# Kernel optimization log

Hardware: AMD Instinct MI355X
Metric: run time of the kernel (lower is better)

## Reference

```python
import jax, jax.numpy as jnp
import numpy as np

N_HEADS = 16
HEAD_DIM = 64
DIM = 1024
B, L = 2, 2048


def setup_inputs() -> dict:
    key = jax.random.key(0)
    ks = jax.random.split(key, 6)
    s = 1.0 / np.sqrt(DIM)
    return {
        "X": jax.random.normal(ks[0], (B, L, DIM), dtype=jnp.float32),
        "attention_mask": jax.random.randint(ks[1], (B, L, L), 0, 2, dtype=jnp.int32),
        "Wq": jax.random.normal(ks[2], (DIM, DIM), dtype=jnp.float32) * s,
        "Wk": jax.random.normal(ks[3], (DIM, DIM), dtype=jnp.float32) * s,
        "Wv": jax.random.normal(ks[4], (DIM, DIM), dtype=jnp.float32) * s,
        "Wo": jax.random.normal(ks[5], (DIM, DIM), dtype=jnp.float32) * s,
    }


def reference(X, attention_mask, Wq, Wk, Wv, Wo):
    # Linear weights follow torch convention: (out_features, in_features)
    b, l, _ = X.shape
    Q = (X @ Wq.T).reshape(b, l, N_HEADS, HEAD_DIM).transpose(0, 2, 1, 3)  # [B,H,L,D]
    K = (X @ Wk.T).reshape(b, l, N_HEADS, HEAD_DIM).transpose(0, 2, 1, 3)
    V = (X @ Wv.T).reshape(b, l, N_HEADS, HEAD_DIM).transpose(0, 2, 1, 3)
    scores = jnp.einsum("bhqd,bhkd->bhqk", Q, K) / np.sqrt(HEAD_DIM)  # [B,H,L,L]
    mask = (attention_mask[:, None, :, :] == 0)  # broadcast over heads
    scores = jnp.where(mask, jnp.float32(-1e20), scores)
    probs = jax.nn.softmax(scores, axis=-1)
    # dropout is identity in eval/inference mode
    ctx = jnp.einsum("bhqk,bhkd->bhqd", probs, V)  # [B,H,L,D]
    ctx = ctx.transpose(0, 2, 1, 3).reshape(b, l, N_HEADS * HEAD_DIM)
    return ctx @ Wo.T
```

## Files before the change

kernel.cpp:

```cpp
#include <hip/hip_runtime.h>
#include <cstddef>


typedef __bf16 bf16x8 __attribute__((ext_vector_type(8)));
typedef __bf16 bf16x4 __attribute__((ext_vector_type(4)));
typedef float  f32x4  __attribute__((ext_vector_type(4)));
typedef short  s16x4  __attribute__((ext_vector_type(4)));

__device__ __forceinline__ void async16(const __bf16* g, __bf16* l) {
  __builtin_amdgcn_global_load_lds((const __attribute__((address_space(1))) unsigned int*)g,
                                   (__attribute__((address_space(3))) unsigned int*)l, 16, 0, 0);
}

__global__ __launch_bounds__(256) void cvt_all(
    const float* __restrict__ X,  const float* __restrict__ Wq, const float* __restrict__ Wk,
    const float* __restrict__ Wv, const float* __restrict__ Wo,
    __bf16* __restrict__ oX,  __bf16* __restrict__ oWq, __bf16* __restrict__ oWk,
    __bf16* __restrict__ oWv, __bf16* __restrict__ oWo) {
  int i = blockIdx.x * 256 + threadIdx.x;
  const float* s; __bf16* d; int off;
  if (i < 1048576)      { s = X;  d = oX;  off = i; }
  else if (i < 1310720) { s = Wq; d = oWq; off = i - 1048576; }
  else if (i < 1572864) { s = Wk; d = oWk; off = i - 1310720; }
  else if (i < 1835008) { s = Wv; d = oWv; off = i - 1572864; }
  else                  { s = Wo; d = oWo; off = i - 1835008; }
  float4 v = ((const float4*)s)[off];
  bf16x4 o;
  o.x = (__bf16)v.x; o.y = (__bf16)v.y; o.z = (__bf16)v.z; o.w = (__bf16)v.w;
  ((bf16x4*)d)[off] = o;
}

__global__ __launch_bounds__(256) void mask_pack(const int* __restrict__ m,
                                                 unsigned long long* __restrict__ pm) {
  int w = blockIdx.x * 4 + (threadIdx.x >> 6);
  int lane = threadIdx.x & 63;
  unsigned long long bits = __ballot(m[(size_t)w * 64 + lane] != 0);
  int b = w >> 16, q = (w >> 5) & 2047, kt = w & 31;
  if (lane == 0) pm[((size_t)b << 16) + kt * 2048 + q] = bits;
}

template<bool OUT_BF16>
__device__ __forceinline__ void gemm128(const __bf16* __restrict__ A, const __bf16* __restrict__ B,
                                        void* __restrict__ C, int lda, int ldb, int ldc,
                                        int m0, int n0, __bf16* As, __bf16* Bs) {
  const int tid = threadIdx.x;
  const int wave = tid >> 6, lane = tid & 63, quad = lane >> 4, l15 = lane & 15;
  const int wm = (wave & 1) * 64, wn = (wave >> 1) * 64;
  const f32x4 z4 = {0.f, 0.f, 0.f, 0.f};
  f32x4 acc[4][4];
#pragma unroll
  for (int i = 0; i < 4; ++i)
#pragma unroll
    for (int j = 0; j < 4; ++j) acc[i][j] = z4;

  for (int k0 = 0; k0 < 1024; k0 += 32) {
#pragma unroll
    for (int s = 0; s < 2; ++s) {
      int p = (wave * 2 + s) * 64 + lane;
      int r = p >> 2;
      int cc = (p & 3) ^ ((r >> 1) & 3);
      async16(A + (size_t)(m0 + r) * lda + (k0 + cc * 8), As + (wave * 2 + s) * 512);
      async16(B + (size_t)(n0 + r) * ldb + (k0 + cc * 8), Bs + (wave * 2 + s) * 512);
    }
    __syncthreads();
    bf16x8 af[4], bfr[4];
#pragma unroll
    for (int i = 0; i < 4; ++i) {
      int r = wm + i * 16 + l15;
      int cc = quad ^ ((r >> 1) & 3);
      af[i] = *(const bf16x8*)(As + r * 32 + cc * 8);
    }
#pragma unroll
    for (int j = 0; j < 4; ++j) {
      int r = wn + j * 16 + l15;
      int cc = quad ^ ((r >> 1) & 3);
      bfr[j] = *(const bf16x8*)(Bs + r * 32 + cc * 8);
    }
#pragma unroll
    for (int i = 0; i < 4; ++i)
#pragma unroll
      for (int j = 0; j < 4; ++j)
        acc[i][j] = __builtin_amdgcn_mfma_f32_16x16x32_bf16(af[i], bfr[j], acc[i][j], 0, 0, 0);
    __syncthreads();
  }
#pragma unroll
  for (int i = 0; i < 4; ++i)
#pragma unroll
    for (int j = 0; j < 4; ++j)
#pragma unroll
      for (int rr = 0; rr < 4; ++rr) {
        int row = m0 + wm + i * 16 + quad * 4 + rr;
        int col = n0 + wn + j * 16 + l15;
        if (OUT_BF16) ((__bf16*)C)[(size_t)row * ldc + col] = (__bf16)acc[i][j][rr];
        else          ((float*)C)[(size_t)row * ldc + col]  = acc[i][j][rr];
      }
}

__global__ __launch_bounds__(256) void qkv_gemm(const __bf16* __restrict__ X,
                                                const __bf16* __restrict__ Wq,
                                                const __bf16* __restrict__ Wk,
                                                const __bf16* __restrict__ Wv,
                                                __bf16* __restrict__ Q, __bf16* __restrict__ K,
                                                __bf16* __restrict__ Vt) {
  __shared__ __bf16 As[4096], Bs[4096];
  int t = blockIdx.x, z = blockIdx.y;
  if (z < 2) {
    int mt = t & 31, nt = t >> 5;
    gemm128<true>(X, z ? Wk : Wq, z ? K : Q, 1024, 1024, 1024, mt * 128, nt * 128, As, Bs);
  } else {
    int mt = t & 7, nt = t >> 3;
    gemm128<true>(Wv, X, Vt, 1024, 1024, 4096, mt * 128, nt * 128, As, Bs);
  }
}

__global__ __launch_bounds__(256) void out_gemm(const __bf16* __restrict__ Ctx,
                                                const __bf16* __restrict__ Wo,
                                                float* __restrict__ Out) {
  __shared__ __bf16 As[4096], Bs[4096];
  int t = blockIdx.x;
  int mt = t & 31, nt = t >> 5;
  gemm128<false>(Ctx, Wo, Out, 1024, 1024, 1024, mt * 128, nt * 128, As, Bs);
}

__global__ __launch_bounds__(256, 2) void attn_kernel(
    const __bf16* __restrict__ Q, const __bf16* __restrict__ K,
    const __bf16* __restrict__ Vt, const unsigned long long* __restrict__ pm,
    __bf16* __restrict__ Ctx) {
  __shared__ __bf16 Ks[2][4096];
  __shared__ __bf16 Vs[2][4096];
  const int tid = threadIdx.x;
  const int wave = tid >> 6, lane = tid & 63, quad = lane >> 4, l15 = lane & 15;
  const int id = blockIdx.x;
  const int qt = id >> 5, hb = id & 31, h = hb & 15, b = hb >> 4;
  const int q0 = qt * 128;
  const int qw = q0 + wave * 32;

  bf16x8 aq[2][2];
#pragma unroll
  for (int st = 0; st < 2; ++st) {
    const __bf16* Qp = Q + (size_t)(b * 2048 + qw + st * 16 + l15) * 1024 + h * 64 + quad * 8;
    aq[st][0] = *(const bf16x8*)Qp;
    aq[st][1] = *(const bf16x8*)(Qp + 32);
  }

  const unsigned long long* Pm = pm + ((size_t)b << 16) + qw + l15;

  auto stage = [&](int buf, int kv0) {
#pragma unroll
    for (int s = 0; s < 2; ++s) {
      int p = s * 256 + wave * 64 + lane;
      int r = p >> 3, c = (p & 7) ^ (r & 7);
      async16(K  + (size_t)(b * 2048 + kv0 + r) * 1024 + h * 64 + c * 8,
              &Ks[buf][(s * 256 + wave * 64) * 8]);
      async16(Vt + (size_t)(h * 64 + r) * 4096 + b * 2048 + kv0 + c * 8,
              &Vs[buf][(s * 256 + wave * 64) * 8]);
    }
  };

  stage(0, 0);
  unsigned long long mw[2] = {Pm[0], Pm[16]};

  const f32x4 z4 = {0.f, 0.f, 0.f, 0.f};
  const short one_bf16 = (short)0x3F80;
  const s16x4 vOnes = {one_bf16, one_bf16, one_bf16, one_bf16};
  f32x4 acc[2][4];
#pragma unroll
  for (int st = 0; st < 2; ++st)
#pragma unroll
    for (int dt = 0; dt < 4; ++dt) acc[st][dt] = z4;
  f32x4 acc_l[2] = {z4, z4};

  for (int t = 0; t < 32; ++t) {
    __syncthreads();
    if (t < 31) stage((t & 1) ^ 1, (t + 1) * 64);

    const __bf16* Kc = Ks[t & 1];
    const __bf16* Vc = Vs[t & 1];

    bf16x8 kA[8];
#pragma unroll
    for (int jt = 0; jt < 4; ++jt) {
      int r = jt * 16 + l15;
      kA[jt * 2]     = *(const bf16x8*)(Kc + r * 64 + ((quad ^ (r & 7)) * 8));
      kA[jt * 2 + 1] = *(const bf16x8*)(Kc + r * 64 + (((4 + quad) ^ (r & 7)) * 8));
    }
    s16x4 vB[4][4];
#pragma unroll
    for (int dt = 0; dt < 4; ++dt) {
      int d = dt * 16 + l15;
#pragma unroll
      for (int kf = 0; kf < 4; ++kf)
        vB[dt][kf] = *(const s16x4*)(Vc + d * 64 + (((kf * 2 + (quad >> 1)) ^ (d & 7)) * 8)
                                     + (quad & 1) * 4);
    }

#pragma unroll
    for (int st = 0; st < 2; ++st) {
      f32x4 s4[4];
#pragma unroll
      for (int jt = 0; jt < 4; ++jt) {
        f32x4 tt = z4;
        tt = __builtin_amdgcn_mfma_f32_16x16x32_bf16(kA[jt * 2],     aq[st][0], tt, 0, 0, 0);
        tt = __builtin_amdgcn_mfma_f32_16x16x32_bf16(kA[jt * 2 + 1], aq[st][1], tt, 0, 0, 0);
        s4[jt] = tt;
      }

      unsigned long long wq = mw[st] >> (quad * 4);
      if (t < 31) mw[st] = Pm[(size_t)(t + 1) * 2048 + st * 16];
      unsigned lo32 = (unsigned)wq, hi32 = (unsigned)(wq >> 32);

#pragma unroll
      for (int kf = 0; kf < 4; ++kf) {
        unsigned bw = (kf < 2) ? lo32 : hi32;
        s16x4 ptk;
#pragma unroll
        for (int rr = 0; rr < 4; ++rr) {
          float e = fmaf(s4[kf][rr], 0.18033688011112042f, -28.853900817779268f);
          e = (bw & (1u << ((kf & 1) * 16 + rr))) ? e : -1e30f;
          float pv = __builtin_amdgcn_exp2f(e);
          ptk[rr] = __builtin_bit_cast(short, (__bf16)pv);
        }
        acc_l[st] = __builtin_amdgcn_mfma_f32_16x16x16bf16_1k(ptk, vOnes, acc_l[st], 0, 0, 0);
#pragma unroll
        for (int dt = 0; dt < 4; ++dt)
          acc[st][dt] = __builtin_amdgcn_mfma_f32_16x16x16bf16_1k(ptk, vB[dt][kf], acc[st][dt], 0, 0, 0);
      }
    }
  }

#pragma unroll
  for (int st = 0; st < 2; ++st) {
    f32x4 inv;
#pragma unroll
    for (int rr = 0; rr < 4; ++rr) inv[rr] = 1.0f / acc_l[st][rr];
#pragma unroll
    for (int dt = 0; dt < 4; ++dt)
#pragma unroll
      for (int rr = 0; rr < 4; ++rr)
        Ctx[(size_t)(b * 2048 + qw + st * 16 + quad * 4 + rr) * 1024 + h * 64 + dt * 16 + l15] =
            (__bf16)(acc[st][dt][rr] * inv[rr]);
  }
}

extern "C" void kernel_launch(void* const* d_in, const int* in_sizes, int n_in,
                              void* d_out, int out_size, void* d_ws, size_t ws_size,
                              hipStream_t stream) {
  const float* X  = (const float*)d_in[0];
  const int* mask = (const int*)d_in[1];
  const float* Wq = (const float*)d_in[2];
  const float* Wk = (const float*)d_in[3];
  const float* Wv = (const float*)d_in[4];
  const float* Wo = (const float*)d_in[5];

  __bf16* w   = (__bf16*)d_ws;
  __bf16* Xbf = w;
  __bf16* Wqb = Xbf + 4194304;
  __bf16* Wkb = Wqb + 1048576;
  __bf16* Wvb = Wkb + 1048576;
  __bf16* Wob = Wvb + 1048576;
  __bf16* Qb  = Wob + 1048576;
  __bf16* Kb  = Qb + 4194304;
  __bf16* Vtb = Kb + 4194304;
  __bf16* Ctx = Vtb + 4194304;
  unsigned long long* pmt = (unsigned long long*)Wqb;

  cvt_all<<<8192, 256, 0, stream>>>(X, Wq, Wk, Wv, Wo, Xbf, Wqb, Wkb, Wvb, Wob);
  qkv_gemm<<<dim3(256, 3), 256, 0, stream>>>(Xbf, Wqb, Wkb, Wvb, Qb, Kb, Vtb);
  mask_pack<<<32768, 256, 0, stream>>>(mask, pmt);
  attn_kernel<<<512, 256, 0, stream>>>(Qb, Kb, Vtb, pmt, Ctx);
  out_gemm<<<256, 256, 0, stream>>>(Ctx, Wob, (float*)d_out);
}
```

Before: 234.6 us.

## Split attention KV range in two blocks and merge partial outputs

Splits each attention block's 2048-key loop into two halves, doubling the grid to 1024 blocks and raising launch bounds to 4 blocks per CU. Each half writes its unnormalized context and row sums, and a new merge kernel adds the halves and normalizes. The softmax scale is folded into Wq during conversion and the exponent bias goes into the MFMA accumulator init, which removes one FMA per score. This trades more parallelism and occupancy for an extra kernel launch, extra global traffic, and bf16 rounding of the partial sums.

```diff
diff --git a/kernel.cpp b/kernel.cpp
--- a/kernel.cpp
+++ b/kernel.cpp
@@ -18,15 +18,16 @@
     __bf16* __restrict__ oX,  __bf16* __restrict__ oWq, __bf16* __restrict__ oWk,
     __bf16* __restrict__ oWv, __bf16* __restrict__ oWo) {
   int i = blockIdx.x * 256 + threadIdx.x;
-  const float* s; __bf16* d; int off;
+  const float* s; __bf16* d; int off; float sc = 1.0f;
   if (i < 1048576)      { s = X;  d = oX;  off = i; }
-  else if (i < 1310720) { s = Wq; d = oWq; off = i - 1048576; }
+  else if (i < 1310720) { s = Wq; d = oWq; off = i - 1048576; sc = 0.18033688011112042f; }
   else if (i < 1572864) { s = Wk; d = oWk; off = i - 1310720; }
   else if (i < 1835008) { s = Wv; d = oWv; off = i - 1572864; }
   else                  { s = Wo; d = oWo; off = i - 1835008; }
   float4 v = ((const float4*)s)[off];
   bf16x4 o;
-  o.x = (__bf16)v.x; o.y = (__bf16)v.y; o.z = (__bf16)v.z; o.w = (__bf16)v.w;
+  o.x = (__bf16)(v.x * sc); o.y = (__bf16)(v.y * sc);
+  o.z = (__bf16)(v.z * sc); o.w = (__bf16)(v.w * sc);
   ((bf16x4*)d)[off] = o;
 }
 
@@ -122,18 +123,20 @@
   gemm128<false>(Ctx, Wo, Out, 1024, 1024, 1024, mt * 128, nt * 128, As, Bs);
 }
 
-__global__ __launch_bounds__(256, 2) void attn_kernel(
+__global__ __launch_bounds__(256, 4) void attn_kernel(
     const __bf16* __restrict__ Q, const __bf16* __restrict__ K,
     const __bf16* __restrict__ Vt, const unsigned long long* __restrict__ pm,
-    __bf16* __restrict__ Ctx) {
+    __bf16* __restrict__ c0, __bf16* __restrict__ c1, float* __restrict__ lp) {
   __shared__ __bf16 Ks[2][4096];
   __shared__ __bf16 Vs[2][4096];
   const int tid = threadIdx.x;
   const int wave = tid >> 6, lane = tid & 63, quad = lane >> 4, l15 = lane & 15;
   const int id = blockIdx.x;
-  const int qt = id >> 5, hb = id & 31, h = hb & 15, b = hb >> 4;
+  const int hb = id & 31, h = hb & 15, b = hb >> 4;
+  const int kvh = (id >> 5) & 1, qt = id >> 6;
   const int q0 = qt * 128;
   const int qw = q0 + wave * 32;
+  const int kt0 = kvh * 16;
 
   bf16x8 aq[2][2];
 #pragma unroll
@@ -157,10 +160,12 @@
     }
   };
 
-  stage(0, 0);
-  unsigned long long mw[2] = {Pm[0], Pm[16]};
+  stage(0, kt0 * 64);
+  unsigned long long mw[2] = {Pm[(size_t)kt0 * 2048], Pm[(size_t)kt0 * 2048 + 16]};
 
   const f32x4 z4 = {0.f, 0.f, 0.f, 0.f};
+  const f32x4 cbias = {-28.853900817779268f, -28.853900817779268f,
+                       -28.853900817779268f, -28.853900817779268f};
   const short one_bf16 = (short)0x3F80;
   const s16x4 vOnes = {one_bf16, one_bf16, one_bf16, one_bf16};
   f32x4 acc[2][4];
@@ -170,9 +175,9 @@
     for (int dt = 0; dt < 4; ++dt) acc[st][dt] = z4;
   f32x4 acc_l[2] = {z4, z4};
 
-  for (int t = 0; t < 32; ++t) {
+  for (int t = 0; t < 16; ++t) {
     __syncthreads();
-    if (t < 31) stage((t & 1) ^ 1, (t + 1) * 64);
+    if (t < 15) stage((t & 1) ^ 1, (kt0 + t + 1) * 64);
 
     const __bf16* Kc = Ks[t & 1];
     const __bf16* Vc = Vs[t & 1];
@@ -199,14 +204,14 @@
       f32x4 s4[4];
 #pragma unroll
       for (int jt = 0; jt < 4; ++jt) {
-        f32x4 tt = z4;
+        f32x4 tt = cbias;
         tt = __builtin_amdgcn_mfma_f32_16x16x32_bf16(kA[jt * 2],     aq[st][0], tt, 0, 0, 0);
         tt = __builtin_amdgcn_mfma_f32_16x16x32_bf16(kA[jt * 2 + 1], aq[st][1], tt, 0, 0, 0);
         s4[jt] = tt;
       }
 
       unsigned long long wq = mw[st] >> (quad * 4);
-      if (t < 31) mw[st] = Pm[(size_t)(t + 1) * 2048 + st * 16];
+      if (t < 15) mw[st] = Pm[(size_t)(kt0 + t + 1) * 2048 + st * 16];
       unsigned lo32 = (unsigned)wq, hi32 = (unsigned)(wq >> 32);
 
 #pragma unroll
@@ -215,8 +220,7 @@
         s16x4 ptk;
 #pragma unroll
         for (int rr = 0; rr < 4; ++rr) {
-          float e = fmaf(s4[kf][rr], 0.18033688011112042f, -28.853900817779268f);
-          e = (bw & (1u << ((kf & 1) * 16 + rr))) ? e : -1e30f;
+          float e = (bw & (1u << ((kf & 1) * 16 + rr))) ? s4[kf][rr] : -1e30f;
           float pv = __builtin_amdgcn_exp2f(e);
           ptk[rr] = __builtin_bit_cast(short, (__bf16)pv);
         }
@@ -228,18 +232,38 @@
     }
   }
 
+  __bf16* cout = kvh ? c1 : c0;
+  float* lout = lp + kvh * 65536;
 #pragma unroll
   for (int st = 0; st < 2; ++st) {
-    f32x4 inv;
-#pragma unroll
-    for (int rr = 0; rr < 4; ++rr) inv[rr] = 1.0f / acc_l[st][rr];
 #pragma unroll
     for (int dt = 0; dt < 4; ++dt)
 #pragma unroll
       for (int rr = 0; rr < 4; ++rr)
-        Ctx[(size_t)(b * 2048 + qw + st * 16 + quad * 4 + rr) * 1024 + h * 64 + dt * 16 + l15] =
-            (__bf16)(acc[st][dt][rr] * inv[rr]);
-  }
+        cout[(size_t)(b * 2048 + qw + st * 16 + quad * 4 + rr) * 1024 + h * 64 + dt * 16 + l15] =
+            (__bf16)acc[st][dt][rr];
+    if (l15 == 0) {
+#pragma unroll
+      for (int rr = 0; rr < 4; ++rr)
+        lout[(size_t)(b * 2048 + qw + st * 16 + quad * 4 + rr) * 16 + h] = acc_l[st][rr];
+    }
+  }
+}
+
+__global__ __launch_bounds__(256) void merge_kernel(const __bf16* __restrict__ c0,
+                                                    const __bf16* __restrict__ c1,
+                                                    const float* __restrict__ lp,
+                                                    __bf16* __restrict__ Ctx) {
+  int i = blockIdx.x * 256 + threadIdx.x;
+  int base = i * 8;
+  int row = base >> 10, h = (base >> 6) & 15;
+  float inv = 1.0f / (lp[row * 16 + h] + lp[65536 + row * 16 + h]);
+  bf16x8 a = ((const bf16x8*)c0)[i];
+  bf16x8 bb = ((const bf16x8*)c1)[i];
+  bf16x8 o;
+#pragma unroll
+  for (int r = 0; r < 8; ++r) o[r] = (__bf16)(((float)a[r] + (float)bb[r]) * inv);
+  ((bf16x8*)Ctx)[i] = o;
 }
 
 extern "C" void kernel_launch(void* const* d_in, const int* in_sizes, int n_in,
@@ -263,10 +287,13 @@
   __bf16* Vtb = Kb + 4194304;
   __bf16* Ctx = Vtb + 4194304;
   unsigned long long* pmt = (unsigned long long*)Wqb;
+  float* lpart = (float*)Wkb;
+  __bf16* c1 = Xbf;
 
   cvt_all<<<8192, 256, 0, stream>>>(X, Wq, Wk, Wv, Wo, Xbf, Wqb, Wkb, Wvb, Wob);
   qkv_gemm<<<dim3(256, 3), 256, 0, stream>>>(Xbf, Wqb, Wkb, Wvb, Qb, Kb, Vtb);
   mask_pack<<<32768, 256, 0, stream>>>(mask, pmt);
-  attn_kernel<<<512, 256, 0, stream>>>(Qb, Kb, Vtb, pmt, Ctx);
+  attn_kernel<<<1024, 256, 0, stream>>>(Qb, Kb, Vtb, pmt, Ctx, c1, lpart);
+  merge_kernel<<<2048, 256, 0, stream>>>(Ctx, c1, lpart, Ctx);
   out_gemm<<<256, 256, 0, stream>>>(Ctx, Wob, (float*)d_out);
 }
```

Measured after the change: 231.2 us. About the same (-1.4%).
